# Kernel optimization log

Measured on AMD Instinct MI355X. Metric: run time of the kernel, lower is better.

## Reference

```python
import jax, jax.numpy as jnp
import numpy as np

B, L, E, H = 4, 1024, 1024, 16
DH = E // H
EPS = 1e-5


def _linear(x, W, b):
    # torch nn.Linear: x @ W.T + b, W: (out, in)
    return jnp.einsum('ble,oe->blo', x, W) + b


def _layernorm(x, g, b):
    m = jnp.mean(x, axis=-1, keepdims=True)
    v = jnp.var(x, axis=-1, keepdims=True)
    return (x - m) * jax.lax.rsqrt(v + EPS) * g + b


def setup_inputs() -> dict:
    key = jax.random.key(0)
    ks = jax.random.split(key, 16)
    s = 1.0 / np.sqrt(E)
    inp = {
        'x': jax.random.normal(ks[0], (B, L, E), dtype=jnp.float32),
        'mask': jax.random.randint(ks[1], (B, L), 0, 2, dtype=jnp.int32),
        'Wq': jax.random.uniform(ks[2], (E, E), jnp.float32, -s, s),
        'bq': jax.random.uniform(ks[3], (E,), jnp.float32, -s, s),
        'Wk': jax.random.uniform(ks[4], (E, E), jnp.float32, -s, s),
        'bk': jax.random.uniform(ks[5], (E,), jnp.float32, -s, s),
        'Wv': jax.random.uniform(ks[6], (E, E), jnp.float32, -s, s),
        'bv': jax.random.uniform(ks[7], (E,), jnp.float32, -s, s),
        'Wo': jax.random.uniform(ks[8], (E, E), jnp.float32, -s, s),
        'bo': jax.random.uniform(ks[9], (E,), jnp.float32, -s, s),
        'g1': jnp.ones((E,), jnp.float32),
        'b1': jnp.zeros((E,), jnp.float32),
        'Wf': jax.random.uniform(ks[10], (E, E), jnp.float32, -s, s),
        'bf': jax.random.uniform(ks[11], (E,), jnp.float32, -s, s),
        'g2': jnp.ones((E,), jnp.float32),
        'b2': jnp.zeros((E,), jnp.float32),
        'alpha': jnp.float32(0.5),
    }
    return inp


def reference(x, mask, Wq, bq, Wk, bk, Wv, bv, Wo, bo, g1, b1, Wf, bf, g2, b2, alpha):
    q = _linear(x, Wq, bq)
    k = _linear(x, Wk, bk)
    v = _linear(x, Wv, bv)
    # Faithful to source: reshape(B, H, L, -1) with NO transpose (non-standard head split)
    q = q.reshape(B, H, L, DH)
    k = k.reshape(B, H, L, DH)
    v = v.reshape(B, H, L, DH)
    scores = jnp.einsum('bhqd,bhkd->bhqk', q, k) / np.sqrt(DH).astype(np.float32)
    # mask (B,L) -> (B,1,1,L), fill -1e10 where mask == 0
    m = mask[:, None, None, :]
    scores = jnp.where(m == 0, jnp.float32(-1e10), scores)
    attn = jax.nn.softmax(scores, axis=-1)
    att = jnp.einsum('bhqk,bhkd->bhqd', attn, v)  # (B,H,L,DH)
    att = att.transpose(0, 2, 1, 3).reshape(B, L, E)
    att = _linear(att, Wo, bo)
    # dropout is identity in eval mode
    skip1 = _layernorm(x + att, g1, b1)
    fcc = jax.nn.gelu(_linear(skip1, Wf, bf), approximate=False)
    skip2 = _layernorm(skip1 + fcc, g2, b2)
    return x * alpha + skip2 * (1.0 - alpha)
```

## Files before the change

### kernel.cpp

```cpp
#include <hip/hip_runtime.h>
#include <hip/hip_bf16.h>
#include <string.h>

typedef __attribute__((ext_vector_type(8))) short short8;
typedef __attribute__((ext_vector_type(4))) float f32x4;
typedef __attribute__((ext_vector_type(4))) unsigned short u16x4;

#define MFMA_BF16(a, b, c) __builtin_amdgcn_mfma_f32_16x16x32_bf16((a), (b), (c), 0, 0, 0)

__device__ __forceinline__ unsigned short f2bf(float f) {
  unsigned int u = __builtin_bit_cast(unsigned int, f);
  u += 0x7fffu + ((u >> 16) & 1u);
  return (unsigned short)(u >> 16);
}

__device__ __forceinline__ float bf2f(unsigned short s) {
  unsigned int u = ((unsigned int)s) << 16;
  return __builtin_bit_cast(float, u);
}

__device__ __forceinline__ unsigned pk_bf16(float a, float b) {
  __hip_bfloat162 h = __float22bfloat162_rn(float2{a, b});
  unsigned r;
  memcpy(&r, &h, 4);
  return r;
}

__device__ __forceinline__ void gload_lds16(const void* g, void* lds) {
  __builtin_amdgcn_global_load_lds(
      (const __attribute__((address_space(1))) unsigned int*)g,
      (__attribute__((address_space(3))) unsigned int*)lds, 16, 0, 0);
}

__global__ __launch_bounds__(256) void cast_all(const float* __restrict__ x,
                                                const float* __restrict__ Wq,
                                                const float* __restrict__ Wk,
                                                const float* __restrict__ Wv,
                                                const float* __restrict__ Wo,
                                                const float* __restrict__ Wf,
                                                unsigned short* __restrict__ xb,
                                                unsigned short* __restrict__ Wqkv,
                                                unsigned short* __restrict__ Wob,
                                                unsigned short* __restrict__ Wfb,
                                                const int* __restrict__ mask,
                                                const float* __restrict__ bq,
                                                const float* __restrict__ bk,
                                                const float* __restrict__ bv,
                                                float* __restrict__ ma,
                                                float* __restrict__ bcat) {
  int i = blockIdx.x * 256 + threadIdx.x;
  if (i < 2359296) {
    const float* src;
    unsigned short* dst;
    int j;
    if (i < 1048576)      { src = x;  dst = xb;             j = i; }
    else if (i < 1310720) { src = Wq; dst = Wqkv;           j = i - 1048576; }
    else if (i < 1572864) { src = Wk; dst = Wqkv + 1048576; j = i - 1310720; }
    else if (i < 1835008) { src = Wv; dst = Wqkv + 2097152; j = i - 1572864; }
    else if (i < 2097152) { src = Wo; dst = Wob;            j = i - 1835008; }
    else                  { src = Wf; dst = Wfb;            j = i - 2097152; }
    float4 v = ((const float4*)src)[j];
    u16x4 r = { f2bf(v.x), f2bf(v.y), f2bf(v.z), f2bf(v.w) };
    ((u16x4*)dst)[j] = r;
  } else {
    int j = i - 2359296;
    if (j < 4096) ma[j] = (mask[j] == 0) ? -1.4426950408889634e10f : 0.0f;
    int k = j - 4096;
    if (k >= 0 && k < 3072) {
      float v = (k < 1024) ? bq[k] : (k < 2048 ? bk[k - 1024] : bv[k - 2048]);
      bcat[k] = v;
    }
  }
}

template <int EPI>
__global__ __launch_bounds__(256) void gemm_lds64(const unsigned short* __restrict__ A,
                                                  const unsigned short* __restrict__ W,
                                                  const float* __restrict__ bias,
                                                  void* __restrict__ Cout,
                                                  int M, int N, int K) {
  __shared__ unsigned short At[128 * 64];
  __shared__ unsigned short Bt[64 * 64];

  const int tid = threadIdx.x;
  const int w = tid >> 6, l = tid & 63;
  const int lr = l & 15, lq = l >> 4;
  const int row0 = blockIdx.x * 128;
  const int col0 = blockIdx.y * 64;

  const int sr8 = l >> 3;
  const int sc8 = ((l & 7) ^ (l >> 3)) * 8;

  f32x4 acc[2][4] = {};

  for (int kt = 0; kt < K; kt += 64) {
#pragma unroll
    for (int j = 0; j < 4; j++) {
      const int r = (w * 4 + j) * 8 + sr8;
      gload_lds16(A + (size_t)(row0 + r) * K + kt + sc8, &At[(w * 4 + j) * 512]);
    }
#pragma unroll
    for (int j = 0; j < 2; j++) {
      const int r = (w * 2 + j) * 8 + sr8;
      gload_lds16(W + (size_t)(col0 + r) * K + kt + sc8, &Bt[(w * 2 + j) * 512]);
    }
    __syncthreads();

    short8 af[2][2], bfr[2][4];
#pragma unroll
    for (int ks = 0; ks < 2; ks++) {
      const int slot = ((ks * 4 + lq) ^ (lr & 7)) * 8;
#pragma unroll
      for (int m = 0; m < 2; m++)
        af[ks][m] = *(const short8*)&At[(w * 32 + m * 16 + lr) * 64 + slot];
#pragma unroll
      for (int n = 0; n < 4; n++)
        bfr[ks][n] = *(const short8*)&Bt[(n * 16 + lr) * 64 + slot];
    }
#pragma unroll
    for (int ks = 0; ks < 2; ks++)
#pragma unroll
      for (int m = 0; m < 2; m++)
#pragma unroll
        for (int n = 0; n < 4; n++)
          acc[m][n] = MFMA_BF16(af[ks][m], bfr[ks][n], acc[m][n]);
    __syncthreads();
  }

#pragma unroll
  for (int n = 0; n < 4; n++) {
    const int col = col0 + n * 16 + lr;
    const float bv = bias[col];
#pragma unroll
    for (int m = 0; m < 2; m++) {
      const int row = row0 + w * 32 + m * 16 + lq * 4;
#pragma unroll
      for (int r = 0; r < 4; r++) {
        float v = acc[m][n][r] + bv;
        if (EPI == 0) {
          ((unsigned short*)Cout)[(size_t)(row + r) * N + col] = f2bf(v);
        } else {
          float g = 0.5f * v * (1.0f + erff(v * 0.70710678118654752f));
          ((unsigned short*)Cout)[(size_t)(row + r) * N + col] = f2bf(g);
        }
      }
    }
  }
}

__global__ __launch_bounds__(256) void vtrans_kernel(const unsigned short* __restrict__ qkv,
                                                     unsigned short* __restrict__ VT) {
  const int bh = blockIdx.x;
  const int kt = blockIdx.y;
  const int t = threadIdx.x;
  const int d = t & 63, kg = t >> 6;
  const unsigned short* basev =
      qkv + ((size_t)(bh >> 4) * 1024 + (bh & 15) * 64) * 3072 + 2048;
  const unsigned short* src = basev + (size_t)(kt * 4 + kg) * 3072 + d;
  unsigned short vals[16];
#pragma unroll
  for (int j = 0; j < 16; j++) vals[j] = src[j * 64];
  short8 v0, v1;
#pragma unroll
  for (int j = 0; j < 8; j++) { v0[j] = (short)vals[j]; v1[j] = (short)vals[8 + j]; }
  size_t dst = ((size_t)bh * 64 + d) * 1024 + kt * 64 + kg * 16;
  *(short8*)&VT[dst] = v0;
  *(short8*)&VT[dst + 8] = v1;
}

__global__ __launch_bounds__(256) void attn13_kernel(const unsigned short* __restrict__ qkv,
                                                     const unsigned short* __restrict__ VT,
                                                     const float* __restrict__ maskadd,
                                                     unsigned short* __restrict__ att) {
  __shared__ unsigned short Kt[2][2048];
  __shared__ unsigned short Vt[2][2048];
  __shared__ float ma_lds[1024];
  __shared__ unsigned short Pl[4][640];

  const int bh = blockIdx.x, b = bh >> 4, h = bh & 15;
  const int qb = blockIdx.y;
  const int tid = threadIdx.x, w = tid >> 6, l = tid & 63;
  const int lr = l & 15, lq = l >> 4;

  const unsigned short* baseq = qkv + ((size_t)b * 1024 + h * 64) * 3072;
  const unsigned short* basek = baseq + 1024;
  const unsigned short* vtb = VT + (size_t)bh * 64 * 1024;

  const int skey = (tid >> 2) & 31;
  const int skd = (tid >> 7) * 32 + (((tid & 3) ^ ((skey >> 1) & 3)) * 8);
  const int svd = tid >> 2;
  const int svc = ((tid & 3) ^ ((svd >> 1) & 3)) * 8;

  ((float4*)ma_lds)[tid] = ((const float4*)(maskadd + b * 1024))[tid];
  {
    gload_lds16(basek + (skey >> 4) * 3072 + (skey & 15) * 64 + skd, (char*)&Kt[0][0] + w * 1024);
    gload_lds16(vtb + (size_t)svd * 1024 + svc, (char*)&Vt[0][0] + w * 1024);
  }

  short8 qf[2];
  const int q0 = qb * 64 + w * 16;
  {
    const int p = q0 + lr;
    const unsigned short* qa = baseq + (p >> 4) * 3072 + (p & 15) * 64;
    qf[0] = *(const short8*)(qa + lq * 8);
    qf[1] = *(const short8*)(qa + 32 + lq * 8);
  }
  __syncthreads();

  float ll = 0.f;
  f32x4 o[4] = {};
  unsigned short* pw = &Pl[w][0];
  constexpr float SC = 0.18033688011112042f;
  const int cx = (lq ^ ((lr >> 1) & 3)) * 8;

  int buf = 0;
#pragma unroll 1
  for (int kt = 0; kt < 32; kt++) {
    if (kt < 31) {
      const int pk = (kt + 1) * 32 + skey;
      gload_lds16(basek + (pk >> 4) * 3072 + (pk & 15) * 64 + skd,
                  (char*)&Kt[buf ^ 1][0] + w * 1024);
      gload_lds16(vtb + (size_t)svd * 1024 + (kt + 1) * 32 + svc,
                  (char*)&Vt[buf ^ 1][0] + w * 1024);
    }

    const unsigned short* KtL = &Kt[buf][0];
    const unsigned short* VtL = &Vt[buf][0];
    short8 vf[4];
#pragma unroll
    for (int n = 0; n < 4; n++)
      vf[n] = *(const short8*)&VtL[(n * 16 + lr) * 32 + cx];

    const float4 mk0 = *(const float4*)&ma_lds[kt * 32 + lq * 4];
    const float4 mk1 = *(const float4*)&ma_lds[kt * 32 + 16 + lq * 4];

    short8 kf00 = *(const short8*)&KtL[lr * 32 + cx];
    short8 kf01 = *(const short8*)&KtL[1024 + lr * 32 + cx];
    short8 kf10 = *(const short8*)&KtL[(16 + lr) * 32 + cx];
    short8 kf11 = *(const short8*)&KtL[1024 + (16 + lr) * 32 + cx];
    f32x4 s0 = {0.f, 0.f, 0.f, 0.f}, s1 = {0.f, 0.f, 0.f, 0.f};
    __builtin_amdgcn_s_setprio(1);
    s0 = MFMA_BF16(kf00, qf[0], s0);
    s0 = MFMA_BF16(kf01, qf[1], s0);
    s1 = MFMA_BF16(kf10, qf[0], s1);
    s1 = MFMA_BF16(kf11, qf[1], s1);
    __builtin_amdgcn_s_setprio(0);

    float p[8], rs = 0.f;
#pragma unroll
    for (int r = 0; r < 4; r++) {
      p[r]     = __builtin_amdgcn_exp2f(s0[r] * SC + ((const float*)&mk0)[r]);
      p[4 + r] = __builtin_amdgcn_exp2f(s1[r] * SC + ((const float*)&mk1)[r]);
    }
#pragma unroll
    for (int i = 0; i < 8; i++) rs += p[i];
    ll += rs;

    uint2 wa, wb;
    wa.x = pk_bf16(p[0], p[1]);
    wa.y = pk_bf16(p[2], p[3]);
    wb.x = pk_bf16(p[4], p[5]);
    wb.y = pk_bf16(p[6], p[7]);
    *(uint2*)&pw[lr * 40 + lq * 4] = wa;
    *(uint2*)&pw[lr * 40 + 16 + lq * 4] = wb;

    asm volatile("s_waitcnt lgkmcnt(0)" ::: "memory");
    const short8 pa = *(const short8*)&pw[lr * 40 + lq * 8];
    __builtin_amdgcn_s_setprio(1);
#pragma unroll
    for (int n = 0; n < 4; n++)
      o[n] = MFMA_BF16(pa, vf[n], o[n]);
    __builtin_amdgcn_s_setprio(0);

    __syncthreads();
    buf ^= 1;
  }

  float lf = ll;
  lf += __shfl_xor(lf, 16);
  lf += __shfl_xor(lf, 32);
  float inv[4];
#pragma unroll
  for (int r = 0; r < 4; r++) inv[r] = 1.0f / __shfl(lf, lq * 4 + r);
#pragma unroll
  for (int r = 0; r < 4; r++) {
    const int q = q0 + lq * 4 + r;
    const size_t obase = ((size_t)b * 1024 + q) * 1024 + h * 64;
#pragma unroll
    for (int n = 0; n < 4; n++)
      att[obase + n * 16 + lr] = f2bf(o[n][r] * inv[r]);
  }
}

__global__ __launch_bounds__(256) void ln1_kernel(const float* __restrict__ x,
                                                  const unsigned short* __restrict__ attp,
                                                  const float* __restrict__ g,
                                                  const float* __restrict__ bt,
                                                  unsigned short* __restrict__ sb) {
  const int row = blockIdx.x, tid = threadIdx.x;
  float4 xv = ((const float4*)(x + row * 1024))[tid];
  u16x4 ab = ((const u16x4*)(attp + row * 1024))[tid];
  float4 v = {xv.x + bf2f(ab[0]), xv.y + bf2f(ab[1]), xv.z + bf2f(ab[2]), xv.w + bf2f(ab[3])};
  float s = v.x + v.y + v.z + v.w;
  float sq = v.x * v.x + v.y * v.y + v.z * v.z + v.w * v.w;
#pragma unroll
  for (int off = 1; off < 64; off <<= 1) { s += __shfl_xor(s, off); sq += __shfl_xor(sq, off); }
  __shared__ float ws[8];
  int wv = tid >> 6, l = tid & 63;
  if (l == 0) { ws[wv] = s; ws[4 + wv] = sq; }
  __syncthreads();
  s = ws[0] + ws[1] + ws[2] + ws[3];
  sq = ws[4] + ws[5] + ws[6] + ws[7];
  float mean = s * (1.0f / 1024.0f);
  float var = sq * (1.0f / 1024.0f) - mean * mean;
  float rs = rsqrtf(var + 1e-5f);
  float4 gv = ((const float4*)g)[tid];
  float4 bv = ((const float4*)bt)[tid];
  u16x4 yb = { f2bf((v.x - mean) * rs * gv.x + bv.x),
               f2bf((v.y - mean) * rs * gv.y + bv.y),
               f2bf((v.z - mean) * rs * gv.z + bv.z),
               f2bf((v.w - mean) * rs * gv.w + bv.w) };
  ((u16x4*)(sb + row * 1024))[tid] = yb;
}

__global__ __launch_bounds__(256) void ln2_kernel(const unsigned short* __restrict__ skip,
                                                  const unsigned short* __restrict__ fcc,
                                                  const float* __restrict__ g,
                                                  const float* __restrict__ bt,
                                                  const float* __restrict__ x,
                                                  const float* __restrict__ alphap,
                                                  float* __restrict__ out) {
  const int row = blockIdx.x, tid = threadIdx.x;
  u16x4 sb = ((const u16x4*)(skip + row * 1024))[tid];
  u16x4 fb = ((const u16x4*)(fcc + row * 1024))[tid];
  float4 v = {bf2f(sb[0]) + bf2f(fb[0]), bf2f(sb[1]) + bf2f(fb[1]),
              bf2f(sb[2]) + bf2f(fb[2]), bf2f(sb[3]) + bf2f(fb[3])};
  float s = v.x + v.y + v.z + v.w;
  float sq = v.x * v.x + v.y * v.y + v.z * v.z + v.w * v.w;
#pragma unroll
  for (int off = 1; off < 64; off <<= 1) { s += __shfl_xor(s, off); sq += __shfl_xor(sq, off); }
  __shared__ float ws[8];
  int wv = tid >> 6, l = tid & 63;
  if (l == 0) { ws[wv] = s; ws[4 + wv] = sq; }
  __syncthreads();
  s = ws[0] + ws[1] + ws[2] + ws[3];
  sq = ws[4] + ws[5] + ws[6] + ws[7];
  float mean = s * (1.0f / 1024.0f);
  float var = sq * (1.0f / 1024.0f) - mean * mean;
  float rs = rsqrtf(var + 1e-5f);
  float4 gv = ((const float4*)g)[tid];
  float4 bv = ((const float4*)bt)[tid];
  float alpha = alphap[0];
  float beta = 1.0f - alpha;
  float4 xv = ((const float4*)(x + row * 1024))[tid];
  float4 y;
  y.x = xv.x * alpha + ((v.x - mean) * rs * gv.x + bv.x) * beta;
  y.y = xv.y * alpha + ((v.y - mean) * rs * gv.y + bv.y) * beta;
  y.z = xv.z * alpha + ((v.z - mean) * rs * gv.z + bv.z) * beta;
  y.w = xv.w * alpha + ((v.w - mean) * rs * gv.w + bv.w) * beta;
  ((float4*)(out + row * 1024))[tid] = y;
}

extern "C" void kernel_launch(void* const* d_in, const int* in_sizes, int n_in,
                              void* d_out, int out_size, void* d_ws, size_t ws_size,
                              hipStream_t stream) {
  const float* x  = (const float*)d_in[0];
  const int* mask = (const int*)d_in[1];
  const float* Wq = (const float*)d_in[2];
  const float* bq = (const float*)d_in[3];
  const float* Wk = (const float*)d_in[4];
  const float* bk = (const float*)d_in[5];
  const float* Wv = (const float*)d_in[6];
  const float* bv = (const float*)d_in[7];
  const float* Wo = (const float*)d_in[8];
  const float* bo = (const float*)d_in[9];
  const float* g1 = (const float*)d_in[10];
  const float* b1 = (const float*)d_in[11];
  const float* Wf = (const float*)d_in[12];
  const float* bf = (const float*)d_in[13];
  const float* g2 = (const float*)d_in[14];
  const float* b2 = (const float*)d_in[15];
  const float* alpha = (const float*)d_in[16];
  float* out = (float*)d_out;

  char* ws = (char*)d_ws;
  size_t off = 0;
  unsigned short* xb   = (unsigned short*)(ws + off); off += 8388608;
  unsigned short* Wqkv = (unsigned short*)(ws + off); off += 6291456;
  unsigned short* Wob  = (unsigned short*)(ws + off); off += 2097152;
  unsigned short* Wfb  = (unsigned short*)(ws + off); off += 2097152;
  float* bcat          = (float*)(ws + off);          off += 12288;
  float* maf           = (float*)(ws + off);          off += 16384;
  unsigned short* qkvb = (unsigned short*)(ws + off); off += 25165824;
  unsigned short* attb = (unsigned short*)(ws + off); off += 8388608;
  float* tmp           = (float*)(ws + off);          off += 16777216;
  unsigned short* s1b  = (unsigned short*)(ws + off); off += 8388608;

  unsigned short* VT  = (unsigned short*)tmp;
  unsigned short* obf = (unsigned short*)tmp;
  unsigned short* fbf = (unsigned short*)tmp + 4194304;

  cast_all<<<9244, 256, 0, stream>>>(x, Wq, Wk, Wv, Wo, Wf, xb, Wqkv, Wob, Wfb,
                                     mask, bq, bk, bv, maf, bcat);

  gemm_lds64<0><<<dim3(32, 48), 256, 0, stream>>>(xb, Wqkv, bcat, qkvb, 4096, 3072, 1024);

  vtrans_kernel<<<dim3(64, 16), 256, 0, stream>>>(qkvb, VT);

  attn13_kernel<<<dim3(64, 16), 256, 0, stream>>>(qkvb, VT, maf, attb);

  gemm_lds64<0><<<dim3(32, 16), 256, 0, stream>>>(attb, Wob, bo, obf, 4096, 1024, 1024);

  ln1_kernel<<<4096, 256, 0, stream>>>(x, obf, g1, b1, s1b);

  gemm_lds64<3><<<dim3(32, 16), 256, 0, stream>>>(s1b, Wfb, bf, fbf, 4096, 1024, 1024);

  ln2_kernel<<<4096, 256, 0, stream>>>(s1b, fbf, g2, b2, x, alpha, out);
}
```

Before: 146.2 us.

## Triple-buffer K/V tiles in attention with prefetch depth two and vmcnt waits

The attention kernel moves from double to triple LDS buffering of K and V tiles and prefetches two tiles ahead. The full __syncthreads is replaced by explicit vmcnt-limited waits plus s_barrier, so a tile's global-to-LDS load can stay in flight across an iteration. The aim is to hide global load latency better. In exchange LDS use goes up by about 8KB per block, which may lower occupancy, and correctness now depends on the hand-counted vmcnt values.

```diff
diff --git a/kernel.cpp b/kernel.cpp
--- a/kernel.cpp
+++ b/kernel.cpp
@@ -168,12 +168,12 @@
   *(short8*)&VT[dst + 8] = v1;
 }
 
-__global__ __launch_bounds__(256) void attn13_kernel(const unsigned short* __restrict__ qkv,
+__global__ __launch_bounds__(256) void attn14_kernel(const unsigned short* __restrict__ qkv,
                                                      const unsigned short* __restrict__ VT,
                                                      const float* __restrict__ maskadd,
                                                      unsigned short* __restrict__ att) {
-  __shared__ unsigned short Kt[2][2048];
-  __shared__ unsigned short Vt[2][2048];
+  __shared__ unsigned short Kt[3][2048];
+  __shared__ unsigned short Vt[3][2048];
   __shared__ float ma_lds[1024];
   __shared__ unsigned short Pl[4][640];
 
@@ -190,12 +190,6 @@
   const int skd = (tid >> 7) * 32 + (((tid & 3) ^ ((skey >> 1) & 3)) * 8);
   const int svd = tid >> 2;
   const int svc = ((tid & 3) ^ ((svd >> 1) & 3)) * 8;
-
-  ((float4*)ma_lds)[tid] = ((const float4*)(maskadd + b * 1024))[tid];
-  {
-    gload_lds16(basek + (skey >> 4) * 3072 + (skey & 15) * 64 + skd, (char*)&Kt[0][0] + w * 1024);
-    gload_lds16(vtb + (size_t)svd * 1024 + svc, (char*)&Vt[0][0] + w * 1024);
-  }
 
   short8 qf[2];
   const int q0 = qb * 64 + w * 16;
@@ -205,7 +199,17 @@
     qf[0] = *(const short8*)(qa + lq * 8);
     qf[1] = *(const short8*)(qa + 32 + lq * 8);
   }
-  __syncthreads();
+  ((float4*)ma_lds)[tid] = ((const float4*)(maskadd + b * 1024))[tid];
+
+#pragma unroll
+  for (int t0 = 0; t0 < 2; t0++) {
+    const int pk = t0 * 32 + skey;
+    gload_lds16(basek + (pk >> 4) * 3072 + (pk & 15) * 64 + skd, (char*)&Kt[t0][0] + w * 1024);
+    gload_lds16(vtb + (size_t)svd * 1024 + t0 * 32 + svc, (char*)&Vt[t0][0] + w * 1024);
+  }
+  asm volatile("s_waitcnt lgkmcnt(0) vmcnt(2)" ::: "memory");
+  __builtin_amdgcn_s_barrier();
+  __builtin_amdgcn_sched_barrier(0);
 
   float ll = 0.f;
   f32x4 o[4] = {};
@@ -213,19 +217,20 @@
   constexpr float SC = 0.18033688011112042f;
   const int cx = (lq ^ ((lr >> 1) & 3)) * 8;
 
-  int buf = 0;
 #pragma unroll 1
   for (int kt = 0; kt < 32; kt++) {
-    if (kt < 31) {
-      const int pk = (kt + 1) * 32 + skey;
+    const int cur = kt % 3;
+    if (kt < 30) {
+      const int st = (kt + 2) % 3;
+      const int pk = (kt + 2) * 32 + skey;
       gload_lds16(basek + (pk >> 4) * 3072 + (pk & 15) * 64 + skd,
-                  (char*)&Kt[buf ^ 1][0] + w * 1024);
-      gload_lds16(vtb + (size_t)svd * 1024 + (kt + 1) * 32 + svc,
-                  (char*)&Vt[buf ^ 1][0] + w * 1024);
-    }
-
-    const unsigned short* KtL = &Kt[buf][0];
-    const unsigned short* VtL = &Vt[buf][0];
+                  (char*)&Kt[st][0] + w * 1024);
+      gload_lds16(vtb + (size_t)svd * 1024 + (kt + 2) * 32 + svc,
+                  (char*)&Vt[st][0] + w * 1024);
+    }
+
+    const unsigned short* KtL = &Kt[cur][0];
+    const unsigned short* VtL = &Vt[cur][0];
     short8 vf[4];
 #pragma unroll
     for (int n = 0; n < 4; n++)
@@ -272,8 +277,15 @@
       o[n] = MFMA_BF16(pa, vf[n], o[n]);
     __builtin_amdgcn_s_setprio(0);
 
-    __syncthreads();
-    buf ^= 1;
+    if (kt < 30) {
+      asm volatile("s_waitcnt vmcnt(2)" ::: "memory");
+      __builtin_amdgcn_s_barrier();
+      __builtin_amdgcn_sched_barrier(0);
+    } else if (kt == 30) {
+      asm volatile("s_waitcnt vmcnt(0)" ::: "memory");
+      __builtin_amdgcn_s_barrier();
+      __builtin_amdgcn_sched_barrier(0);
+    }
   }
 
   float lf = ll;
@@ -407,7 +419,7 @@
 
   vtrans_kernel<<<dim3(64, 16), 256, 0, stream>>>(qkvb, VT);
 
-  attn13_kernel<<<dim3(64, 16), 256, 0, stream>>>(qkvb, VT, maf, attb);
+  attn14_kernel<<<dim3(64, 16), 256, 0, stream>>>(qkvb, VT, maf, attb);
 
   gemm_lds64<0><<<dim3(32, 16), 256, 0, stream>>>(attb, Wob, bo, obf, 4096, 1024, 1024);
 
```

Result: no change. 144.1 us (-1.5%).
